# Kernel tuning notes

Hardware: AMD Instinct MI355X
Metric: run time of the kernel (lower is better)

Reference implementation:

```python
import jax, jax.numpy as jnp
import numpy as np
import math

B, C, H, W = 8, 256, 64, 64
KEYDIM, VALDIM = 128, 256


def conv3x3(x, w, b):
    # x: [B,C,H,W], w: [O,C,3,3] -> [B,O,H,W], SAME padding (padding=1)
    y = jax.lax.conv_general_dilated(x, w, window_strides=(1, 1), padding='SAME',
                                     dimension_numbers=('NCHW', 'OIHW', 'NCHW'))
    return y + b[None, :, None, None]


def setup_inputs() -> dict:
    key = jax.random.key(0)
    ks = jax.random.split(key, 5)
    x = jax.random.normal(ks[0], (B, C, H, W), dtype=jnp.float32)
    fan_in = C * 9
    s = 1.0 / np.sqrt(fan_in)
    key_w = jax.random.uniform(ks[1], (KEYDIM, C, 3, 3), jnp.float32, -s, s)
    key_b = jax.random.uniform(ks[2], (KEYDIM,), jnp.float32, -s, s)
    val_w = jax.random.uniform(ks[3], (VALDIM, C, 3, 3), jnp.float32, -s, s)
    val_b = jax.random.uniform(ks[4], (VALDIM,), jnp.float32, -s, s)
    return {"x": x, "key_w": key_w, "key_b": key_b, "val_w": val_w, "val_b": val_b}


def reference(x, key_w, key_b, val_w, val_b):
    b_, c_, h_, w_ = x.shape
    k = conv3x3(x, key_w, key_b).reshape(b_, KEYDIM, h_ * w_)   # [B,K,N]
    v = conv3x3(x, val_w, val_b)                                 # [B,V,H,W]
    sq = jnp.sum(k * k, axis=1)                                  # [B,N]
    a = sq[:, :, None]                                           # [B,N,1]
    c2 = sq[:, None, :]                                          # [B,1,N]
    dots = 2.0 * jnp.einsum('bki,bkj->bij', k, k)                # [B,N,N]
    affinity = (-a + dots - c2) / math.sqrt(KEYDIM)              # -||ki-kj||^2 / sqrt(K)
    affinity = jax.nn.softmax(affinity, axis=1)                  # softmax over dim=1 (rows)
    self_attn = jnp.einsum('bvi,bij->bvj', v.reshape(b_, VALDIM, h_ * w_), affinity)
    self_attn = self_attn.reshape(b_, VALDIM, h_, w_)
    return jnp.concatenate((v, self_attn), axis=1)               # [B,2V,H,W]
```

## Files before the change

### kernel.cpp

```cpp
#include <hip/hip_runtime.h>
#include <hip/hip_bf16.h>
#include <cstdint>

constexpr int Bb = 8, Cc = 256, Hh = 64, Ww = 64, Nn = 4096;
constexpr int KD = 128, VD = 256, HP = 66;

typedef __attribute__((ext_vector_type(8))) short short8_t;
typedef __attribute__((ext_vector_type(4))) short shortx4;
typedef __attribute__((ext_vector_type(4))) float floatx4;

static __device__ __forceinline__ ushort f2bf(float f) {
    union { float f; uint32_t u; } v{f};
    uint32_t r = v.u + 0x7FFFu + ((v.u >> 16) & 1u);
    return (ushort)(r >> 16);
}
static __device__ __forceinline__ float bf2f(ushort b) {
    union { uint32_t u; float f; } v{(uint32_t)b << 16};
    return v.f;
}

static __device__ __forceinline__ void gload_lds16(const void* g, void* l) {
    __builtin_amdgcn_global_load_lds((const __attribute__((address_space(1))) uint32_t*)g,
                                     (__attribute__((address_space(3))) uint32_t*)l, 16, 0, 0);
}

__global__ __launch_bounds__(256) void pad_transpose(const float* __restrict__ x,
                                                     ushort* __restrict__ xpad) {
    int bid = blockIdx.x;
    int b = bid & 7, rest = bid >> 3;
    int y = rest & 63, cg = rest >> 6;
    int t = threadIdx.x;
    __shared__ float tile[64][65];
    int xcol = t & 63;
    int crow = t >> 6;
    const float* xb = x + ((size_t)(b * Cc + cg * 64) * Nn) + y * 64;
#pragma unroll
    for (int i = 0; i < 16; i++) {
        int c = crow + i * 4;
        tile[c][xcol] = xb[(size_t)c * Nn + xcol];
    }
    __syncthreads();
    int c = t & 63;
    int x4 = t >> 6;
    ushort* dst = xpad + (((size_t)(b * HP + (y + 1)) * HP) + 1) * Cc + cg * 64 + c;
#pragma unroll
    for (int i = 0; i < 16; i++) {
        int xx = x4 + i * 4;
        dst[(size_t)xx * Cc] = f2bf(tile[c][xx]);
    }
}

__global__ __launch_bounds__(256) void repack_w(const float* __restrict__ kw,
                                                const float* __restrict__ vw,
                                                ushort* __restrict__ wtk,
                                                ushort* __restrict__ wtv) {
    int idx = blockIdx.x * 256 + threadIdx.x;
    const int nk = KD * Cc;
    const int nv = VD * Cc;
    if (idx < nk) {
        const float* src = kw + (size_t)idx * 9;
        int oc = idx / Cc, c = idx % Cc;
#pragma unroll
        for (int r = 0; r < 9; r++) wtk[((size_t)r * KD + oc) * Cc + c] = f2bf(src[r]);
    } else if (idx < nk + nv) {
        int j = idx - nk;
        const float* src = vw + (size_t)j * 9;
        int oc = j / Cc, c = j % Cc;
#pragma unroll
        for (int r = 0; r < 9; r++) wtv[((size_t)r * VD + oc) * Cc + c] = f2bf(src[r]);
    }
}

template <int MODE, int OC>
__global__ __launch_bounds__(256) void conv_gemm(const ushort* __restrict__ xpad,
                                                 const ushort* __restrict__ wt,
                                                 const float* __restrict__ bias,
                                                 ushort* __restrict__ kt_out,
                                                 float* __restrict__ f32_out,
                                                 ushort* __restrict__ vb_out) {
    int bid = blockIdx.x;
    int b = bid & 7;
    int ocg, y;
    if (OC == 128) { ocg = 0; y = bid >> 3; }
    else           { ocg = (bid >> 3) & 1; y = bid >> 4; }
    int lane = threadIdx.x & 63, wv = threadIdx.x >> 6;
    int l15 = lane & 15, g = lane >> 4;
    int oc0 = ocg * 128;
    const int swzA = l15 & 7;

    __shared__ ushort wslab[2][128 * 128];

    size_t wsoff[8];
    int ldsrow[8];
#pragma unroll
    for (int h = 0; h < 8; h++) {
        int row = wv * 32 + h * 4 + (lane >> 4);
        wsoff[h] = (size_t)row * Cc + (((lane & 15) ^ (row & 7)) * 8);
        ldsrow[h] = (wv * 32 + h * 4) * 128;
    }

    floatx4 acc[8];
#pragma unroll
    for (int m = 0; m < 8; m++) acc[m] = (floatx4){0.f, 0.f, 0.f, 0.f};

    const ushort* xb = xpad + ((size_t)b * HP * HP) * Cc;
    int xcol = wv * 16 + l15;

    auto stage = [&](int hs, int bi) {
        int r = hs >> 1, hc = hs & 1;
        const ushort* wb = wt + ((size_t)r * OC + oc0) * Cc + hc * 128;
#pragma unroll
        for (int h = 0; h < 8; h++)
            gload_lds16(wb + wsoff[h], &wslab[bi][ldsrow[h]]);
    };

    stage(0, 0);
    __syncthreads();

#pragma unroll 1
    for (int hs = 0; hs < 18; ++hs) {
        int bi = hs & 1;
        if (hs < 17) stage(hs + 1, bi ^ 1);

        int r = hs >> 1, hc = hs & 1;
        int dy = r / 3, dx = r % 3;
        const ushort* bsrc = xb + ((size_t)(y + dy) * HP + xcol + dx) * Cc + hc * 128 + g * 8;
#pragma unroll
        for (int cc = 0; cc < 4; cc++) {
            short8_t bfrag = *(const short8_t*)(bsrc + cc * 32);
#pragma unroll
            for (int m = 0; m < 8; m++) {
                short8_t afrag = *(const short8_t*)&wslab[bi][(m * 16 + l15) * 128 + ((cc * 4 + g) ^ swzA) * 8];
                acc[m] = __builtin_amdgcn_mfma_f32_16x16x32_bf16(afrag, bfrag, acc[m], 0, 0, 0);
            }
        }
        __syncthreads();
    }

    int pos = y * 64 + xcol;
    if (MODE == 0) {
        ushort* kt = kt_out + ((size_t)(b * Nn + pos)) * KD;
#pragma unroll
        for (int m = 0; m < 8; m++) {
            floatx4 bv = *(const floatx4*)(bias + m * 16 + g * 4);
            shortx4 pk;
#pragma unroll
            for (int r = 0; r < 4; r++) pk[r] = (short)f2bf(acc[m][r] + bv[r]);
            *(shortx4*)(kt + m * 16 + g * 4) = pk;
        }
    } else {
#pragma unroll
        for (int m = 0; m < 8; m++) {
            floatx4 bv = *(const floatx4*)(bias + oc0 + m * 16 + g * 4);
#pragma unroll
            for (int r = 0; r < 4; r++) {
                int oc = oc0 + m * 16 + g * 4 + r;
                float v = acc[m][r] + bv[r];
                f32_out[((size_t)(b * 512 + oc)) * Nn + pos] = v;
                vb_out[((size_t)(b * VD + oc)) * Nn + pos] = f2bf(v);
            }
        }
    }
}

__global__ __launch_bounds__(256) void sq_kernel(const ushort* __restrict__ kt,
                                                 float* __restrict__ sq) {
    int bid = blockIdx.x;
    int idx = (bid & 7) * Nn + (bid >> 3) * 256 + threadIdx.x;
    const ushort* src = kt + (size_t)idx * KD;
    float s = 0.f;
#pragma unroll
    for (int i = 0; i < 16; i++) {
        short8_t v = *(const short8_t*)(src + i * 8);
#pragma unroll
        for (int e = 0; e < 8; e++) {
            float f = bf2f((ushort)v[e]);
            s += f * f;
        }
    }
    sq[idx] = s;
}

__global__ __launch_bounds__(256) void attn_kernel(const ushort* __restrict__ kt,
                                                   const ushort* __restrict__ vb,
                                                   const float* __restrict__ sq,
                                                   float* __restrict__ out) {
    int bid = blockIdx.x;
    int b = bid & 7, jt = bid >> 3;
    int lane = threadIdx.x & 63, wv = threadIdx.x >> 6;
    int l15 = lane & 15, g = lane >> 4;

    __shared__ ushort bufK[64 * 128];
    __shared__ ushort bufV[256 * 64];
    __shared__ ushort pt[4][16][72];

    int j = jt * 64 + wv * 16 + l15;
    const ushort* ktb = kt + ((size_t)b * Nn) * KD;
    const ushort* vbb = vb + ((size_t)b * VD) * Nn;
    const float* sqb = sq + b * Nn;

    const ushort* skp[4];
#pragma unroll
    for (int h = 0; h < 4; h++) {
        int row = wv * 16 + h * 4 + (lane >> 4);
        skp[h] = ktb + (size_t)row * KD + (((lane & 15) ^ (row & 7)) * 8);
    }
    const ushort* svp[8];
#pragma unroll
    for (int h = 0; h < 8; h++) {
        int vd = wv * 64 + h * 8 + (lane >> 3);
        svp[h] = vbb + (size_t)vd * Nn + (((lane & 7) ^ (vd & 7)) * 8);
    }

    float sqj = sqb[j];
    short8_t kj[4];
#pragma unroll
    for (int kk = 0; kk < 4; kk++)
        kj[kk] = *(const short8_t*)(ktb + (size_t)j * KD + kk * 32 + g * 8);

    floatx4 acc[16];
#pragma unroll
    for (int m = 0; m < 16; m++) acc[m] = (floatx4){0.f, 0.f, 0.f, 0.f};
    float dsum = 0.f;
    constexpr float kScale = 0.08838834764831845f * 1.4426950408889634f;
    const int swzA = l15 & 7;

#pragma unroll
    for (int h = 0; h < 4; h++) gload_lds16(skp[h], &bufK[(wv * 16 + h * 4) * 128]);
#pragma unroll
    for (int h = 0; h < 8; h++) gload_lds16(svp[h], &bufV[(wv * 64 + h * 8) * 64]);
    __syncthreads();

#pragma unroll 1
    for (int it = 0; it < 64; ++it) {
        int i0 = it * 64;

        floatx4 sacc[4];
#pragma unroll
        for (int f = 0; f < 4; f++) sacc[f] = (floatx4){0.f, 0.f, 0.f, 0.f};
#pragma unroll
        for (int kk = 0; kk < 4; kk++) {
#pragma unroll
            for (int f = 0; f < 4; f++) {
                short8_t afr = *(const short8_t*)&bufK[(f * 16 + l15) * 128 + ((kk * 4 + g) ^ swzA) * 8];
                sacc[f] = __builtin_amdgcn_mfma_f32_16x16x32_bf16(afr, kj[kk], sacc[f], 0, 0, 0);
            }
        }
#pragma unroll
        for (int f = 0; f < 4; f++) {
            shortx4 pk;
#pragma unroll
            for (int r = 0; r < 4; r++) {
                int ii = i0 + f * 16 + g * 4 + r;
                float p = exp2f((2.f * sacc[f][r] - sqb[ii] - sqj) * kScale);
                dsum += p;
                pk[r] = (short)f2bf(p);
            }
            *(shortx4*)&pt[wv][l15][f * 16 + g * 4] = pk;
        }
        __syncthreads();

        if (it < 63) {
#pragma unroll
            for (int h = 0; h < 4; h++)
                gload_lds16(skp[h] + (size_t)(i0 + 64) * KD, &bufK[(wv * 16 + h * 4) * 128]);
        }

#pragma unroll
        for (int k2 = 0; k2 < 2; k2++) {
            short8_t pfr = *(const short8_t*)&pt[wv][l15][k2 * 32 + g * 8];
#pragma unroll
            for (int m = 0; m < 16; m++) {
                short8_t vfr = *(const short8_t*)&bufV[(m * 16 + l15) * 64 + ((k2 * 4 + g) ^ swzA) * 8];
                acc[m] = __builtin_amdgcn_mfma_f32_16x16x32_bf16(vfr, pfr, acc[m], 0, 0, 0);
            }
        }
        __syncthreads();

        if (it < 63) {
#pragma unroll
            for (int h = 0; h < 8; h++)
                gload_lds16(svp[h] + (i0 + 64), &bufV[(wv * 64 + h * 8) * 64]);
        }
    }

    dsum += __shfl_xor(dsum, 16, 64);
    dsum += __shfl_xor(dsum, 32, 64);
    float rden = 1.f / dsum;

    float* ob = out + ((size_t)(b * 512 + 256)) * Nn + j;
#pragma unroll
    for (int m = 0; m < 16; m++) {
#pragma unroll
        for (int r = 0; r < 4; r++) {
            int vd = m * 16 + g * 4 + r;
            ob[(size_t)vd * Nn] = acc[m][r] * rden;
        }
    }
}

extern "C" void kernel_launch(void* const* d_in, const int* in_sizes, int n_in,
                              void* d_out, int out_size, void* d_ws, size_t ws_size,
                              hipStream_t stream) {
    const float* x     = (const float*)d_in[0];
    const float* kw    = (const float*)d_in[1];
    const float* kbias = (const float*)d_in[2];
    const float* vw    = (const float*)d_in[3];
    const float* vbias = (const float*)d_in[4];
    float* out = (float*)d_out;
    char* ws = (char*)d_ws;

    constexpr size_t XPAD = 0;
    constexpr size_t WTK  = 17842176;
    constexpr size_t WTV  = 18432000;
    constexpr size_t KT   = 19611648;
    constexpr size_t VB   = 28000256;
    constexpr size_t SQ   = 44777472;

    ushort* xpad = (ushort*)(ws + XPAD);
    ushort* wtk  = (ushort*)(ws + WTK);
    ushort* wtv  = (ushort*)(ws + WTV);
    ushort* ktw  = (ushort*)(ws + KT);
    ushort* vbw  = (ushort*)(ws + VB);
    float*  sqw  = (float*)(ws + SQ);

    hipMemsetAsync(xpad, 0, 17842176, stream);
    pad_transpose<<<dim3(2048), 256, 0, stream>>>(x, xpad);
    repack_w<<<dim3(384), 256, 0, stream>>>(kw, vw, wtk, wtv);
    conv_gemm<0, KD><<<dim3(512), 256, 0, stream>>>(xpad, wtk, kbias, ktw, nullptr, nullptr);
    conv_gemm<1, VD><<<dim3(1024), 256, 0, stream>>>(xpad, wtv, vbias, nullptr, out, vbw);
    sq_kernel<<<dim3(128), 256, 0, stream>>>(ktw, sqw);
    attn_kernel<<<dim3(512), 256, 0, stream>>>(ktw, vbw, sqw, out);
}
```

Measured before the change: 277.1 us.

## Re-partition attention waves to split i-rows and V-rows across a 64-column tile

Each wave now computes scores for 16 i-rows against all 64 j-columns and accumulates a 64×64 slice of V-dims across those columns, instead of owning 16 j-columns against everything. This cuts the LDS reads of K and V fragments per MFMA, since each A fragment is reused across four B fragments. Softmax denominators now need a cross-wave LDS reduction at the end. The scale is folded into sq in the precompute kernel, and a packed bf16 convert instruction replaces the manual rounding.

```diff
diff --git a/kernel.cpp b/kernel.cpp
--- a/kernel.cpp
+++ b/kernel.cpp
@@ -8,6 +8,9 @@
 typedef __attribute__((ext_vector_type(8))) short short8_t;
 typedef __attribute__((ext_vector_type(4))) short shortx4;
 typedef __attribute__((ext_vector_type(4))) float floatx4;
+
+constexpr float kScale = 0.08838834764831845f * 1.4426950408889634f;
+constexpr float kTwoK  = 2.0f * kScale;
 
 static __device__ __forceinline__ ushort f2bf(float f) {
     union { float f; uint32_t u; } v{f};
@@ -17,6 +20,11 @@
 static __device__ __forceinline__ float bf2f(ushort b) {
     union { uint32_t u; float f; } v{(uint32_t)b << 16};
     return v.f;
+}
+static __device__ __forceinline__ uint32_t pk_bf16(float a, float b) {
+    uint32_t r;
+    asm("v_cvt_pk_bf16_f32 %0, %1, %2" : "=v"(r) : "v"(a), "v"(b));
+    return r;
 }
 
 static __device__ __forceinline__ void gload_lds16(const void* g, void* l) {
@@ -178,12 +186,12 @@
             s += f * f;
         }
     }
-    sq[idx] = s;
+    sq[idx] = s * kScale;
 }
 
 __global__ __launch_bounds__(256) void attn_kernel(const ushort* __restrict__ kt,
                                                    const ushort* __restrict__ vb,
-                                                   const float* __restrict__ sq,
+                                                   const float* __restrict__ sq2,
                                                    float* __restrict__ out) {
     int bid = blockIdx.x;
     int b = bid & 7, jt = bid >> 3;
@@ -192,12 +200,12 @@
 
     __shared__ ushort bufK[64 * 128];
     __shared__ ushort bufV[256 * 64];
-    __shared__ ushort pt[4][16][72];
-
-    int j = jt * 64 + wv * 16 + l15;
+    __shared__ ushort pt[64][72];
+    __shared__ float pdsum[4][4][16];
+
     const ushort* ktb = kt + ((size_t)b * Nn) * KD;
     const ushort* vbb = vb + ((size_t)b * VD) * Nn;
-    const float* sqb = sq + b * Nn;
+    const float* sqb = sq2 + b * Nn;
 
     const ushort* skp[4];
 #pragma unroll
@@ -212,17 +220,23 @@
         svp[h] = vbb + (size_t)vd * Nn + (((lane & 7) ^ (vd & 7)) * 8);
     }
 
-    float sqj = sqb[j];
-    short8_t kj[4];
-#pragma unroll
-    for (int kk = 0; kk < 4; kk++)
-        kj[kk] = *(const short8_t*)(ktb + (size_t)j * KD + kk * 32 + g * 8);
-
-    floatx4 acc[16];
-#pragma unroll
-    for (int m = 0; m < 16; m++) acc[m] = (floatx4){0.f, 0.f, 0.f, 0.f};
-    float dsum = 0.f;
-    constexpr float kScale = 0.08838834764831845f * 1.4426950408889634f;
+    short8_t kj[4][4];
+    float sq2j[4];
+#pragma unroll
+    for (int s = 0; s < 4; s++) {
+        int j = jt * 64 + s * 16 + l15;
+        sq2j[s] = sqb[j];
+#pragma unroll
+        for (int kk = 0; kk < 4; kk++)
+            kj[s][kk] = *(const short8_t*)(ktb + (size_t)j * KD + kk * 32 + g * 8);
+    }
+
+    floatx4 acc[4][4];
+#pragma unroll
+    for (int m = 0; m < 4; m++)
+#pragma unroll
+        for (int s = 0; s < 4; s++) acc[m][s] = (floatx4){0.f, 0.f, 0.f, 0.f};
+    float dsumv[4] = {0.f, 0.f, 0.f, 0.f};
     const int swzA = l15 & 7;
 
 #pragma unroll
@@ -237,26 +251,24 @@
 
         floatx4 sacc[4];
 #pragma unroll
-        for (int f = 0; f < 4; f++) sacc[f] = (floatx4){0.f, 0.f, 0.f, 0.f};
+        for (int s = 0; s < 4; s++) sacc[s] = (floatx4){0.f, 0.f, 0.f, 0.f};
 #pragma unroll
         for (int kk = 0; kk < 4; kk++) {
-#pragma unroll
-            for (int f = 0; f < 4; f++) {
-                short8_t afr = *(const short8_t*)&bufK[(f * 16 + l15) * 128 + ((kk * 4 + g) ^ swzA) * 8];
-                sacc[f] = __builtin_amdgcn_mfma_f32_16x16x32_bf16(afr, kj[kk], sacc[f], 0, 0, 0);
-            }
-        }
-#pragma unroll
-        for (int f = 0; f < 4; f++) {
-            shortx4 pk;
-#pragma unroll
-            for (int r = 0; r < 4; r++) {
-                int ii = i0 + f * 16 + g * 4 + r;
-                float p = exp2f((2.f * sacc[f][r] - sqb[ii] - sqj) * kScale);
-                dsum += p;
-                pk[r] = (short)f2bf(p);
-            }
-            *(shortx4*)&pt[wv][l15][f * 16 + g * 4] = pk;
+            short8_t afr = *(const short8_t*)&bufK[(wv * 16 + l15) * 128 + ((kk * 4 + g) ^ swzA) * 8];
+#pragma unroll
+            for (int s = 0; s < 4; s++)
+                sacc[s] = __builtin_amdgcn_mfma_f32_16x16x32_bf16(afr, kj[s][kk], sacc[s], 0, 0, 0);
+        }
+        floatx4 sqi = *(const floatx4*)(sqb + i0 + wv * 16 + g * 4);
+#pragma unroll
+        for (int s = 0; s < 4; s++) {
+            float p0 = exp2f(sacc[s][0] * kTwoK - sqi[0] - sq2j[s]);
+            float p1 = exp2f(sacc[s][1] * kTwoK - sqi[1] - sq2j[s]);
+            float p2 = exp2f(sacc[s][2] * kTwoK - sqi[2] - sq2j[s]);
+            float p3 = exp2f(sacc[s][3] * kTwoK - sqi[3] - sq2j[s]);
+            dsumv[s] += (p0 + p1) + (p2 + p3);
+            uint2 w2 = {pk_bf16(p0, p1), pk_bf16(p2, p3)};
+            *(uint2*)&pt[s * 16 + l15][wv * 16 + g * 4] = w2;
         }
         __syncthreads();
 
@@ -268,11 +280,17 @@
 
 #pragma unroll
         for (int k2 = 0; k2 < 2; k2++) {
-            short8_t pfr = *(const short8_t*)&pt[wv][l15][k2 * 32 + g * 8];
-#pragma unroll
-            for (int m = 0; m < 16; m++) {
-                short8_t vfr = *(const short8_t*)&bufV[(m * 16 + l15) * 64 + ((k2 * 4 + g) ^ swzA) * 8];
-                acc[m] = __builtin_amdgcn_mfma_f32_16x16x32_bf16(vfr, pfr, acc[m], 0, 0, 0);
+            short8_t pfr[4];
+#pragma unroll
+            for (int s = 0; s < 4; s++)
+                pfr[s] = *(const short8_t*)&pt[s * 16 + l15][k2 * 32 + g * 8];
+#pragma unroll
+            for (int m = 0; m < 4; m++) {
+                int row = wv * 64 + m * 16 + l15;
+                short8_t vfr = *(const short8_t*)&bufV[row * 64 + ((k2 * 4 + g) ^ swzA) * 8];
+#pragma unroll
+                for (int s = 0; s < 4; s++)
+                    acc[m][s] = __builtin_amdgcn_mfma_f32_16x16x32_bf16(vfr, pfr[s], acc[m][s], 0, 0, 0);
             }
         }
         __syncthreads();
@@ -284,17 +302,32 @@
         }
     }
 
-    dsum += __shfl_xor(dsum, 16, 64);
-    dsum += __shfl_xor(dsum, 32, 64);
-    float rden = 1.f / dsum;
-
-    float* ob = out + ((size_t)(b * 512 + 256)) * Nn + j;
-#pragma unroll
-    for (int m = 0; m < 16; m++) {
-#pragma unroll
-        for (int r = 0; r < 4; r++) {
-            int vd = m * 16 + g * 4 + r;
-            ob[(size_t)vd * Nn] = acc[m][r] * rden;
+#pragma unroll
+    for (int s = 0; s < 4; s++) {
+        dsumv[s] += __shfl_xor(dsumv[s], 16, 64);
+        dsumv[s] += __shfl_xor(dsumv[s], 32, 64);
+    }
+    if (g == 0) {
+#pragma unroll
+        for (int s = 0; s < 4; s++) pdsum[wv][s][l15] = dsumv[s];
+    }
+    __syncthreads();
+    float rden[4];
+#pragma unroll
+    for (int s = 0; s < 4; s++)
+        rden[s] = 1.f / (((pdsum[0][s][l15] + pdsum[1][s][l15]) +
+                          (pdsum[2][s][l15] + pdsum[3][s][l15])));
+
+    float* ob = out + ((size_t)(b * 512 + 256 + wv * 64)) * Nn + jt * 64 + l15;
+#pragma unroll
+    for (int m = 0; m < 4; m++) {
+#pragma unroll
+        for (int s = 0; s < 4; s++) {
+#pragma unroll
+            for (int r = 0; r < 4; r++) {
+                int vd = m * 16 + g * 4 + r;
+                ob[(size_t)vd * Nn + s * 16] = acc[m][s][r] * rden[s];
+            }
         }
     }
 }
```

New measurement: 341.4 us. 23.2% more time.

## Double-buffer K/V tiles in attention loop with one barrier per step

Applied to the files above, without the earlier changes.

The attention kernel now walks the key dimension in 32-row tiles held in two LDS buffers. The loads for the next tile are issued at the top of each step, so they overlap with the current step's MFMA work, and each iteration needs only one barrier instead of two. The exponent is simplified as well: the per-column squared norm cancels in the column softmax and is dropped, the row norms are prescaled in sq_kernel, and probabilities are packed with v_cvt_pk_bf16_f32. Dropping the column norm removes the guarantee that the exponent stays non-positive, which adds some risk of overflow for large key norms, and the smaller tiles mean more loop iterations.

```diff
diff --git a/kernel.cpp b/kernel.cpp
--- a/kernel.cpp
+++ b/kernel.cpp
@@ -8,6 +8,9 @@
 typedef __attribute__((ext_vector_type(8))) short short8_t;
 typedef __attribute__((ext_vector_type(4))) short shortx4;
 typedef __attribute__((ext_vector_type(4))) float floatx4;
+
+constexpr float kScale = 0.08838834764831845f * 1.4426950408889634f;
+constexpr float kTwoK  = 2.0f * kScale;
 
 static __device__ __forceinline__ ushort f2bf(float f) {
     union { float f; uint32_t u; } v{f};
@@ -17,6 +20,11 @@
 static __device__ __forceinline__ float bf2f(ushort b) {
     union { uint32_t u; float f; } v{(uint32_t)b << 16};
     return v.f;
+}
+static __device__ __forceinline__ uint32_t pk_bf16(float a, float b) {
+    uint32_t r;
+    asm("v_cvt_pk_bf16_f32 %0, %1, %2" : "=v"(r) : "v"(a), "v"(b));
+    return r;
 }
 
 static __device__ __forceinline__ void gload_lds16(const void* g, void* l) {
@@ -178,41 +186,44 @@
             s += f * f;
         }
     }
-    sq[idx] = s;
+    sq[idx] = s * kScale;
 }
 
 __global__ __launch_bounds__(256) void attn_kernel(const ushort* __restrict__ kt,
                                                    const ushort* __restrict__ vb,
-                                                   const float* __restrict__ sq,
+                                                   const float* __restrict__ sq2,
                                                    float* __restrict__ out) {
     int bid = blockIdx.x;
     int b = bid & 7, jt = bid >> 3;
     int lane = threadIdx.x & 63, wv = threadIdx.x >> 6;
     int l15 = lane & 15, g = lane >> 4;
 
-    __shared__ ushort bufK[64 * 128];
-    __shared__ ushort bufV[256 * 64];
-    __shared__ ushort pt[4][16][72];
-
-    int j = jt * 64 + wv * 16 + l15;
+    __shared__ ushort bufK[2][32 * 128];
+    __shared__ ushort bufV[2][256 * 32];
+    __shared__ ushort pt[4][16][36];
+
     const ushort* ktb = kt + ((size_t)b * Nn) * KD;
     const ushort* vbb = vb + ((size_t)b * VD) * Nn;
-    const float* sqb = sq + b * Nn;
-
-    const ushort* skp[4];
+    const float* sqb = sq2 + b * Nn;
+
+    const ushort* skp[2];
+    int skrow[2];
+#pragma unroll
+    for (int h = 0; h < 2; h++) {
+        int row = wv * 8 + h * 4 + (lane >> 4);
+        skrow[h] = (wv * 8 + h * 4) * 128;
+        skp[h] = ktb + (size_t)row * KD + (((lane & 15) ^ (row & 7)) * 8);
+    }
+    const ushort* svp[4];
+    int svrow[4];
 #pragma unroll
     for (int h = 0; h < 4; h++) {
-        int row = wv * 16 + h * 4 + (lane >> 4);
-        skp[h] = ktb + (size_t)row * KD + (((lane & 15) ^ (row & 7)) * 8);
-    }
-    const ushort* svp[8];
-#pragma unroll
-    for (int h = 0; h < 8; h++) {
-        int vd = wv * 64 + h * 8 + (lane >> 3);
-        svp[h] = vbb + (size_t)vd * Nn + (((lane & 7) ^ (vd & 7)) * 8);
-    }
-
-    float sqj = sqb[j];
+        int vd = wv * 64 + h * 16 + (lane >> 2);
+        svrow[h] = (wv * 64 + h * 16) * 32;
+        svp[h] = vbb + (size_t)vd * Nn + (((lane & 3) ^ (vd & 3)) * 8);
+    }
+
+    int j = jt * 64 + wv * 16 + l15;
     short8_t kj[4];
 #pragma unroll
     for (int kk = 0; kk < 4; kk++)
@@ -222,66 +233,60 @@
 #pragma unroll
     for (int m = 0; m < 16; m++) acc[m] = (floatx4){0.f, 0.f, 0.f, 0.f};
     float dsum = 0.f;
-    constexpr float kScale = 0.08838834764831845f * 1.4426950408889634f;
     const int swzA = l15 & 7;
 
 #pragma unroll
-    for (int h = 0; h < 4; h++) gload_lds16(skp[h], &bufK[(wv * 16 + h * 4) * 128]);
-#pragma unroll
-    for (int h = 0; h < 8; h++) gload_lds16(svp[h], &bufV[(wv * 64 + h * 8) * 64]);
+    for (int h = 0; h < 2; h++) gload_lds16(skp[h], &bufK[0][skrow[h]]);
+#pragma unroll
+    for (int h = 0; h < 4; h++) gload_lds16(svp[h], &bufV[0][svrow[h]]);
     __syncthreads();
 
 #pragma unroll 1
-    for (int it = 0; it < 64; ++it) {
-        int i0 = it * 64;
-
-        floatx4 sacc[4];
-#pragma unroll
-        for (int f = 0; f < 4; f++) sacc[f] = (floatx4){0.f, 0.f, 0.f, 0.f};
+    for (int it = 0; it < 128; ++it) {
+        int i0 = it * 32;
+        int cur = it & 1;
+
+        if (it < 127) {
+#pragma unroll
+            for (int h = 0; h < 2; h++)
+                gload_lds16(skp[h] + (size_t)(i0 + 32) * KD, &bufK[cur ^ 1][skrow[h]]);
+#pragma unroll
+            for (int h = 0; h < 4; h++)
+                gload_lds16(svp[h] + (i0 + 32), &bufV[cur ^ 1][svrow[h]]);
+        }
+
+        floatx4 sacc[2];
+#pragma unroll
+        for (int f = 0; f < 2; f++) sacc[f] = (floatx4){0.f, 0.f, 0.f, 0.f};
 #pragma unroll
         for (int kk = 0; kk < 4; kk++) {
 #pragma unroll
-            for (int f = 0; f < 4; f++) {
-                short8_t afr = *(const short8_t*)&bufK[(f * 16 + l15) * 128 + ((kk * 4 + g) ^ swzA) * 8];
+            for (int f = 0; f < 2; f++) {
+                short8_t afr = *(const short8_t*)&bufK[cur][(f * 16 + l15) * 128 + ((kk * 4 + g) ^ swzA) * 8];
                 sacc[f] = __builtin_amdgcn_mfma_f32_16x16x32_bf16(afr, kj[kk], sacc[f], 0, 0, 0);
             }
         }
 #pragma unroll
-        for (int f = 0; f < 4; f++) {
-            shortx4 pk;
-#pragma unroll
-            for (int r = 0; r < 4; r++) {
-                int ii = i0 + f * 16 + g * 4 + r;
-                float p = exp2f((2.f * sacc[f][r] - sqb[ii] - sqj) * kScale);
-                dsum += p;
-                pk[r] = (short)f2bf(p);
-            }
-            *(shortx4*)&pt[wv][l15][f * 16 + g * 4] = pk;
-        }
+        for (int f = 0; f < 2; f++) {
+            floatx4 sqi = *(const floatx4*)(sqb + i0 + f * 16 + g * 4);
+            float p0 = exp2f(sacc[f][0] * kTwoK - sqi[0]);
+            float p1 = exp2f(sacc[f][1] * kTwoK - sqi[1]);
+            float p2 = exp2f(sacc[f][2] * kTwoK - sqi[2]);
+            float p3 = exp2f(sacc[f][3] * kTwoK - sqi[3]);
+            dsum += (p0 + p1) + (p2 + p3);
+            uint2 w2 = {pk_bf16(p0, p1), pk_bf16(p2, p3)};
+            *(uint2*)&pt[wv][l15][f * 16 + g * 4] = w2;
+        }
+
+        short8_t pfr = *(const short8_t*)&pt[wv][l15][g * 8];
+#pragma unroll
+        for (int m = 0; m < 16; m++) {
+            int row = m * 16 + l15;
+            short8_t vfr = *(const short8_t*)&bufV[cur][row * 32 + (g ^ (row & 3)) * 8];
+            acc[m] = __builtin_amdgcn_mfma_f32_16x16x32_bf16(vfr, pfr, acc[m], 0, 0, 0);
+        }
+
         __syncthreads();
-
-        if (it < 63) {
-#pragma unroll
-            for (int h = 0; h < 4; h++)
-                gload_lds16(skp[h] + (size_t)(i0 + 64) * KD, &bufK[(wv * 16 + h * 4) * 128]);
-        }
-
-#pragma unroll
-        for (int k2 = 0; k2 < 2; k2++) {
-            short8_t pfr = *(const short8_t*)&pt[wv][l15][k2 * 32 + g * 8];
-#pragma unroll
-            for (int m = 0; m < 16; m++) {
-                short8_t vfr = *(const short8_t*)&bufV[(m * 16 + l15) * 64 + ((k2 * 4 + g) ^ swzA) * 8];
-                acc[m] = __builtin_amdgcn_mfma_f32_16x16x32_bf16(vfr, pfr, acc[m], 0, 0, 0);
-            }
-        }
-        __syncthreads();
-
-        if (it < 63) {
-#pragma unroll
-            for (int h = 0; h < 8; h++)
-                gload_lds16(svp[h] + (i0 + 64), &bufV[(wv * 64 + h * 8) * 64]);
-        }
     }
 
     dsum += __shfl_xor(dsum, 16, 64);
```

After: 327.7 us. 1.18x slower.
